# Performance work log

Measured on AMD Instinct MI355X. Metric: run time of the kernel, lower is better.

Reference implementation:

```python
import jax, jax.numpy as jnp
import numpy as np

KS = 3
N = KS * KS  # 9 kernel taps
EPS = 1e-5
LEAK = 0.1


def _conv2d(x, w, b=None, stride=1, pad=1):
    out = jax.lax.conv_general_dilated(
        x, w, (stride, stride), [(pad, pad), (pad, pad)],
        dimension_numbers=('NCHW', 'OIHW', 'NCHW'))
    if b is not None:
        out = out + b[None, :, None, None]
    return out


def setup_inputs() -> dict:
    key = jax.random.key(0)
    k1, k2, k3, k4 = jax.random.split(key, 4)
    b, c_in, c_out, H, W = 4, 128, 256, 128, 128
    x = jax.random.normal(k1, (b, c_in, H, W), dtype=jnp.float32)
    # offset-predicting conv (torch inits it to zero; small random keeps
    # sampling near-grid but nontrivial)
    p_w = jax.random.normal(k2, (2 * N, c_in, KS, KS), dtype=jnp.float32) * 0.01
    p_b = jnp.zeros((2 * N,), dtype=jnp.float32)
    # main conv weight (bias=False in DeformConv2d)
    w_conv = jax.random.normal(k3, (c_out, c_in, KS, KS), dtype=jnp.float32) * 0.05
    gamma = jnp.ones((c_out,), dtype=jnp.float32)
    beta = jnp.zeros((c_out,), dtype=jnp.float32)
    return {"x": x, "p_w": p_w, "p_b": p_b, "w_conv": w_conv,
            "gamma": gamma, "beta": beta}


def reference(x, p_w, p_b, w_conv, gamma, beta):
    b, c, H, W = x.shape
    # offsets: (b, 2N, H, W); first N channels = x-offsets, last N = y-offsets
    off = jnp.transpose(_conv2d(x, p_w, p_b), (0, 2, 3, 1))  # (b,h,w,2N)
    off_x, off_y = off[..., :N], off[..., N:]

    x_pad = jnp.pad(x, ((0, 0), (0, 0), (1, 1), (1, 1)))  # zero_padding(1)
    Hp, Wp = H + 2, W + 2

    # p = p_0 + p_n + offset (in padded coordinates)
    dx = jnp.repeat(jnp.arange(-1, 2), KS).astype(x.dtype)  # (9,)
    dy = jnp.tile(jnp.arange(-1, 2), KS).astype(x.dtype)
    p0x = jnp.arange(1, H + 1, dtype=x.dtype)[None, :, None, None]
    p0y = jnp.arange(1, W + 1, dtype=x.dtype)[None, None, :, None]
    px = p0x + dx + off_x  # (b,h,w,N)
    py = p0y + dy + off_y

    fx, fy = jnp.floor(px), jnp.floor(py)
    qlt_x = jnp.clip(fx, 0, Hp - 1)
    qlt_y = jnp.clip(fy, 0, Wp - 1)
    qrb_x = jnp.clip(fx + 1, 0, Hp - 1)
    qrb_y = jnp.clip(fy + 1, 0, Wp - 1)

    pcx = jnp.clip(px, 0, Hp - 1)
    pcy = jnp.clip(py, 0, Wp - 1)

    # bilinear weights (matches original g_lt/g_rb/g_lb/g_rt)
    g_lt = (1 + (qlt_x - pcx)) * (1 + (qlt_y - pcy))
    g_rb = (1 - (qrb_x - pcx)) * (1 - (qrb_y - pcy))
    g_lb = (1 + (qlt_x - pcx)) * (1 - (qrb_y - pcy))
    g_rt = (1 - (qrb_x - pcx)) * (1 + (qlt_y - pcy))

    x_flat = x_pad.reshape(b, c, Hp * Wp)
    ilt_x, ilt_y = qlt_x.astype(jnp.int32), qlt_y.astype(jnp.int32)
    irb_x, irb_y = qrb_x.astype(jnp.int32), qrb_y.astype(jnp.int32)

    def samp(ix, iy, g):
        idx = (ix * Wp + iy).reshape(b, -1)  # (b, h*w*N)
        v = jnp.take_along_axis(x_flat, idx[:, None, :], axis=2)
        return g[:, None] * v.reshape(b, c, H, W, N)

    x_off = (samp(ilt_x, ilt_y, g_lt) + samp(irb_x, irb_y, g_rb)
             + samp(ilt_x, irb_y, g_lb) + samp(irb_x, ilt_y, g_rt))

    # equivalent to reshaping to (b,c,3h,3w) and conv(k=3,s=3), bias=False
    out = jnp.einsum('bchwn,ocn->bohw', x_off,
                     w_conv.reshape(w_conv.shape[0], c, N))

    # BatchNorm2d (training-mode batch stats, biased var) + LeakyReLU(0.1)
    mean = out.mean(axis=(0, 2, 3), keepdims=True)
    var = ((out - mean) ** 2).mean(axis=(0, 2, 3), keepdims=True)
    out = (out - mean) * jax.lax.rsqrt(var + EPS)
    out = out * gamma[None, :, None, None] + beta[None, :, None, None]
    return jnp.where(out >= 0, out, LEAK * out)
```

## Files before the change

kernel.cpp:

```cpp
#include <hip/hip_runtime.h>
#include <cstdint>

typedef __attribute__((ext_vector_type(8))) short bf16x8;
typedef __attribute__((ext_vector_type(4))) float f32x4;

#define B_   4
#define C_   128
#define H_   128
#define W_   128
#define HP_  130
#define WP_  130
#define O_   256
#define HW_  (H_*W_)

#define XPAD_BYTES   (B_*HP_*WP_*C_*2)
#define OFF_BYTE     XPAD_BYTES
#define OFF_BYTES    (B_*HW_*18*4)
#define WREPB_BYTE   (OFF_BYTE + OFF_BYTES)
#define WREPB_BYTES  (9*C_*O_*2)
#define STATS_BYTE   (WREPB_BYTE + WREPB_BYTES)
#define WOFF_BYTE    (STATS_BYTE + 4096)
#define WOFF_BYTES   (9*4*4*32*8*2)
#define RAW_BYTE     (WOFF_BYTE + WOFF_BYTES)
#define RAW_BYTES    ((size_t)B_*O_*HW_*2)
#define WS_NEED      ((size_t)RAW_BYTE + RAW_BYTES)

typedef __attribute__((address_space(1))) const void gconst_void;
typedef __attribute__((address_space(3))) void lds_void;
#define GLD_LDS16(gp, lp) __builtin_amdgcn_global_load_lds((gconst_void*)(gp), (lds_void*)(lp), 16, 0, 0)

__device__ __forceinline__ unsigned pack_bf2(float a, float b) {
    unsigned ua = __builtin_bit_cast(unsigned, a) + 0x8000u;
    unsigned ub = __builtin_bit_cast(unsigned, b) + 0x8000u;
    return __builtin_amdgcn_perm(ub, ua, 0x07060302u);
}

__device__ __forceinline__ unsigned short bf16_rne(float f) {
    unsigned u = __builtin_bit_cast(unsigned, f);
    u += 0x7fffu + ((u >> 16) & 1u);
    return (unsigned short)(u >> 16);
}

__global__ void k_transpose(const float* __restrict__ x, unsigned short* __restrict__ xpad,
                            const float* __restrict__ p_w, short* __restrict__ wofff,
                            const float* __restrict__ w_conv, unsigned short* __restrict__ wrepb,
                            float* __restrict__ stats) {
    __shared__ float tile[32][33];
    int w0 = blockIdx.x * 32, c0 = blockIdx.y * 32;
    int bh = blockIdx.z;
    int b = bh >> 7, h = bh & 127;
    int tx = threadIdx.x, ty = threadIdx.y;
#pragma unroll
    for (int i = 0; i < 4; i++) {
        int c = c0 + ty + i * 8;
        tile[ty + i * 8][tx] = x[((b * C_ + c) * H_ + h) * W_ + w0 + tx];
    }
    int tid = ty * 32 + tx;
    {
        int fb = (bh * 4 + (int)blockIdx.y) * 4 + (int)blockIdx.x;
        int i = fb * 256 + tid;
        if (i < 1024) stats[i] = 0.f;
        if (i < 9 * 4096) {
            int e = i & 7, m = (i >> 3) & 31, q = (i >> 8) & 3, kc = (i >> 10) & 3, tap = i >> 12;
            float f = (m < 18) ? p_w[((size_t)m * C_ + kc * 32 + q * 8 + e) * 9 + tap] : 0.f;
            wofff[i] = (short)bf16_rne(f);
        }
        int j = i - 9 * 4096;
        if (j >= 0 && j < 9 * C_ * O_) {
            int ki8 = j & 7;
            int o   = (j >> 3) & 255;
            int kq  = (j >> 11) & 3;
            int kc  = (j >> 13) & 3;
            int n   = j >> 15;
            int c = kc * 32 + kq * 8 + ki8;
            wrepb[j] = bf16_rne(w_conv[(o * C_ + c) * 9 + n]);
        }
    }
    if (h == 0) {
        int wloc = tid >> 3, cq = tid & 7;
        size_t r0 = ((size_t)(b * HP_ + 0)   * WP_ + (w0 + 1 + wloc)) * C_ + c0 + cq * 4;
        size_t r1 = ((size_t)(b * HP_ + 129) * WP_ + (w0 + 1 + wloc)) * C_ + c0 + cq * 4;
        *(uint2*)&xpad[r0] = make_uint2(0u, 0u);
        *(uint2*)&xpad[r1] = make_uint2(0u, 0u);
        if (w0 == 0 && tid < 128) {
            int corner = tid >> 5, cc = tid & 31;
            int hp = (corner & 1) ? 129 : 0;
            int wp = (corner & 2) ? 129 : 0;
            xpad[((size_t)(b * HP_ + hp) * WP_ + wp) * C_ + c0 + cc] = 0;
        }
    }
    if (w0 == 0 && tid < 64) {
        int side = tid >> 5, cc = tid & 31;
        int wp = side ? 129 : 0;
        xpad[((size_t)(b * HP_ + h + 1) * WP_ + wp) * C_ + c0 + cc] = 0;
    }
    __syncthreads();
    if (tid < 128) {
        int w = tid >> 2, u4 = tid & 3;
        unsigned r0 = pack_bf2(tile[8 * u4 + 0][w], tile[8 * u4 + 1][w]);
        unsigned r1 = pack_bf2(tile[8 * u4 + 2][w], tile[8 * u4 + 3][w]);
        unsigned r2 = pack_bf2(tile[8 * u4 + 4][w], tile[8 * u4 + 5][w]);
        unsigned r3 = pack_bf2(tile[8 * u4 + 6][w], tile[8 * u4 + 7][w]);
        *(uint4*)&xpad[((size_t)((b * HP_ + h + 1) * WP_ + (w0 + w + 1))) * C_ + c0 + u4 * 8] =
            make_uint4(r0, r1, r2, r3);
    }
}

__global__ __launch_bounds__(256) void k_offconv(const unsigned short* __restrict__ xpad,
                                                 const short* __restrict__ wofff,
                                                 const float* __restrict__ p_b,
                                                 float* __restrict__ offT) {
    int t = threadIdx.x;
    int ph = blockIdx.x;
    int h  = blockIdx.y;
    int b  = blockIdx.z;
    const unsigned short* xb = xpad + (size_t)b * HP_ * WP_ * C_;
    int lane = t & 63, wv = t >> 6;
    int q = lane >> 4, l15 = lane & 15;
    int pos0 = ph * 64 + wv * 16;
    int poscol = pos0 + l15;

    f32x4 accA = {0.f, 0.f, 0.f, 0.f}, accB = {0.f, 0.f, 0.f, 0.f};
    const bf16x8* Wf = (const bf16x8*)wofff;

    for (int tap = 0; tap < 9; tap++) {
        int row = h + tap / 3;
        int col = poscol + tap % 3;
        const unsigned short* src = xb + ((size_t)(row * WP_ + col)) * C_ + q * 8;
#pragma unroll
        for (int kc = 0; kc < 4; kc++) {
            bf16x8 a0 = Wf[(size_t)(((tap * 4 + kc) * 4 + q) * 32) + l15];
            bf16x8 a1 = Wf[(size_t)(((tap * 4 + kc) * 4 + q) * 32) + 16 + l15];
            bf16x8 bv = *(const bf16x8*)(src + kc * 32);
            accA = __builtin_amdgcn_mfma_f32_16x16x32_bf16(a0, bv, accA, 0, 0, 0);
            accB = __builtin_amdgcn_mfma_f32_16x16x32_bf16(a1, bv, accB, 0, 0, 0);
        }
    }
    size_t hw = (size_t)h * W_ + pos0 + l15;
#pragma unroll
    for (int r = 0; r < 4; r++) {
        int j = q * 4 + r;
        offT[((size_t)(b * 18 + j)) * HW_ + hw] = accA[r] + p_b[j];
    }
    if (q == 0) {
#pragma unroll
        for (int r = 0; r < 2; r++) {
            int j = 16 + r;
            offT[((size_t)(b * 18 + j)) * HW_ + hw] = accB[r] + p_b[j];
        }
    }
}

__global__ __launch_bounds__(512, 4) void k_main(const unsigned short* __restrict__ xpad,
                                                 const float* __restrict__ offT,
                                                 const unsigned short* __restrict__ wrepb,
                                                 float* __restrict__ out,
                                                 float* __restrict__ stats,
                                                 unsigned short* __restrict__ rawout,
                                                 int bf16flag) {
    __shared__ short Wl[2][8192];
    __shared__ short Vl[2][4128];
    __shared__ int   pbase[2][4][128];
    __shared__ float pg[2][4][128];
    __shared__ float red0[256], red1[256];

    int t = threadIdx.x;
    int i_blk = blockIdx.x;
    int b = i_blk & 3;
    int h = i_blk >> 2;
    const unsigned short* xb = xpad + (size_t)b * HP_ * WP_ * C_;

    int lane = t & 63, wv = t >> 6;
    int q = lane >> 4, l15 = lane & 15;
    int m0 = (wv & 3) * 64;
    int ph = wv >> 2;
    int n0 = ph * 64;
    int c4g = t & 3, posb = t >> 2;

    auto OFFSETS = [&](int n, int pb) {
        if (t < 128) {
            int w = t;
            float offx = offT[((size_t)(b * 18 + n)) * HW_ + h * W_ + w];
            float offy = offT[((size_t)(b * 18 + 9 + n)) * HW_ + h * W_ + w];
            int dxn = n / 3 - 1, dyn = n % 3 - 1;
            float px = (float)(h + 1 + dxn) + offx;
            float py = (float)(w + 1 + dyn) + offy;
            float pcx = fminf(fmaxf(px, 0.f), 129.f);
            float pcy = fminf(fmaxf(py, 0.f), 129.f);
            float fx = floorf(px), fy = floorf(py);
            float q0x = fminf(fmaxf(fx, 0.f), 129.f);
            float q0y = fminf(fmaxf(fy, 0.f), 129.f);
            float q1x = fminf(fmaxf(fx + 1.f, 0.f), 129.f);
            float q1y = fminf(fmaxf(fy + 1.f, 0.f), 129.f);
            float wx0 = 1.f + (q0x - pcx), wx1 = 1.f - (q1x - pcx);
            float wy0 = 1.f + (q0y - pcy), wy1 = 1.f - (q1y - pcy);
            int i0x = (int)q0x, i0y = (int)q0y, i1x = (int)q1x, i1y = (int)q1y;
            pbase[pb][0][w] = (i0x * WP_ + i0y) * C_;
            pbase[pb][1][w] = (i1x * WP_ + i1y) * C_;
            pbase[pb][2][w] = (i0x * WP_ + i1y) * C_;
            pbase[pb][3][w] = (i1x * WP_ + i0y) * C_;
            pg[pb][0][w] = wx0 * wy0;
            pg[pb][1][w] = wx1 * wy1;
            pg[pb][2][w] = wx0 * wy1;
            pg[pb][3][w] = wx1 * wy0;
        }
    };

    f32x4 acc[4][4];
#pragma unroll
    for (int i = 0; i < 4; i++)
#pragma unroll
        for (int j = 0; j < 4; j++) acc[i][j] = (f32x4){0.f, 0.f, 0.f, 0.f};

    if (t < 256) { red0[t] = 0.f; red1[t] = 0.f; }
    OFFSETS(0, 0);
    __syncthreads();

    {
        const unsigned short* ws = wrepb;
        GLD_LDS16(ws + (size_t)t * 8, &Wl[0][wv * 512]);
        GLD_LDS16(ws + (size_t)(t + 512) * 8, &Wl[0][wv * 512 + 4096]);
        int cof = c4g * 8;
        uint4 A  = *(const uint4*)(xb + pbase[0][0][posb] + cof);
        uint4 Bv = *(const uint4*)(xb + pbase[0][1][posb] + cof);
        uint4 Cv = *(const uint4*)(xb + pbase[0][2][posb] + cof);
        uint4 Dv = *(const uint4*)(xb + pbase[0][3][posb] + cof);
        float g0 = pg[0][0][posb], g1 = pg[0][1][posb], g2 = pg[0][2][posb], g3 = pg[0][3][posb];
        unsigned outw[4];
#pragma unroll
        for (int k = 0; k < 4; k++) {
            unsigned ua = (&A.x)[k], ub = (&Bv.x)[k], uc = (&Cv.x)[k], ud = (&Dv.x)[k];
            float alo = __builtin_bit_cast(float, ua << 16), ahi = __builtin_bit_cast(float, ua & 0xffff0000u);
            float blo = __builtin_bit_cast(float, ub << 16), bhi = __builtin_bit_cast(float, ub & 0xffff0000u);
            float clo = __builtin_bit_cast(float, uc << 16), chi = __builtin_bit_cast(float, uc & 0xffff0000u);
            float dlo = __builtin_bit_cast(float, ud << 16), dhi = __builtin_bit_cast(float, ud & 0xffff0000u);
            float vlo = g0 * alo + g1 * blo + g2 * clo + g3 * dlo;
            float vhi = g0 * ahi + g1 * bhi + g2 * chi + g3 * dhi;
            outw[k] = pack_bf2(vlo, vhi);
        }
        *(uint4*)&Vl[0][(unsigned)(c4g * 129 + posb) * 8] = make_uint4(outw[0], outw[1], outw[2], outw[3]);
    }
    __syncthreads();

#pragma unroll 1
    for (int s = 0; s < 36; s++) {
        int cur = s & 1, nxt = cur ^ 1;
        uint4 A, Bv, Cv, Dv;
        float g0 = 0.f, g1 = 0.f, g2 = 0.f, g3 = 0.f;
        bool st = (s < 35);
        if (st) {
            int s1 = s + 1;
            const unsigned short* ws = wrepb + (size_t)s1 * 8192;
            GLD_LDS16(ws + (size_t)t * 8, &Wl[nxt][wv * 512]);
            GLD_LDS16(ws + (size_t)(t + 512) * 8, &Wl[nxt][wv * 512 + 4096]);
            int n1 = s1 >> 2, kc1 = s1 & 3, pb1 = n1 & 1;
            int cof = kc1 * 32 + c4g * 8;
            A  = *(const uint4*)(xb + pbase[pb1][0][posb] + cof);
            Bv = *(const uint4*)(xb + pbase[pb1][1][posb] + cof);
            Cv = *(const uint4*)(xb + pbase[pb1][2][posb] + cof);
            Dv = *(const uint4*)(xb + pbase[pb1][3][posb] + cof);
            g0 = pg[pb1][0][posb]; g1 = pg[pb1][1][posb];
            g2 = pg[pb1][2][posb]; g3 = pg[pb1][3][posb];
        }
        {
            const bf16x8* Af = (const bf16x8*)Wl[cur];
            const bf16x8* Bf = (const bf16x8*)Vl[cur];
            bf16x8 av[4];
#pragma unroll
            for (int i = 0; i < 4; i++) av[i] = Af[q * 256 + m0 + i * 16 + l15];
            __builtin_amdgcn_s_setprio(1);
#pragma unroll
            for (int j = 0; j < 4; j++) {
                bf16x8 bv = Bf[q * 129 + n0 + j * 16 + l15];
#pragma unroll
                for (int i = 0; i < 4; i++)
                    acc[i][j] = __builtin_amdgcn_mfma_f32_16x16x32_bf16(av[i], bv, acc[i][j], 0, 0, 0);
            }
            __builtin_amdgcn_s_setprio(0);
        }
        if ((s & 3) == 2) {
            int n = s >> 2;
            if (n < 8) OFFSETS(n + 1, (n + 1) & 1);
        }
        if (st) {
            unsigned outw[4];
#pragma unroll
            for (int k = 0; k < 4; k++) {
                unsigned ua = (&A.x)[k], ub = (&Bv.x)[k], uc = (&Cv.x)[k], ud = (&Dv.x)[k];
                float alo = __builtin_bit_cast(float, ua << 16), ahi = __builtin_bit_cast(float, ua & 0xffff0000u);
                float blo = __builtin_bit_cast(float, ub << 16), bhi = __builtin_bit_cast(float, ub & 0xffff0000u);
                float clo = __builtin_bit_cast(float, uc << 16), chi = __builtin_bit_cast(float, uc & 0xffff0000u);
                float dlo = __builtin_bit_cast(float, ud << 16), dhi = __builtin_bit_cast(float, ud & 0xffff0000u);
                float vlo = g0 * alo + g1 * blo + g2 * clo + g3 * dlo;
                float vhi = g0 * ahi + g1 * bhi + g2 * chi + g3 * dhi;
                outw[k] = pack_bf2(vlo, vhi);
            }
            *(uint4*)&Vl[nxt][(unsigned)(c4g * 129 + posb) * 8] = make_uint4(outw[0], outw[1], outw[2], outw[3]);
        }
        __syncthreads();
    }

#pragma unroll
    for (int i = 0; i < 4; i++) {
#pragma unroll
        for (int r = 0; r < 4; r++) {
            int o_loc = m0 + i * 16 + q * 4 + r;
            float s = 0.f, s2 = 0.f;
#pragma unroll
            for (int j = 0; j < 4; j++) { float v = acc[i][j][r]; s += v; s2 += v * v; }
            s  += __shfl_xor(s, 1);  s  += __shfl_xor(s, 2);  s  += __shfl_xor(s, 4);  s  += __shfl_xor(s, 8);
            s2 += __shfl_xor(s2, 1); s2 += __shfl_xor(s2, 2); s2 += __shfl_xor(s2, 4); s2 += __shfl_xor(s2, 8);
            if (l15 == 0) { atomicAdd(&red0[o_loc], s); atomicAdd(&red1[o_loc], s2); }
        }
    }
    __syncthreads();
    if (t < 256) {
        atomicAdd(&stats[t], red0[t]);
        atomicAdd(&stats[256 + t], red1[t]);
    }

    if (bf16flag) {
        unsigned short* rb = rawout + ((size_t)b * O_) * HW_ + (size_t)h * W_;
#pragma unroll
        for (int i = 0; i < 4; i++)
#pragma unroll
            for (int j = 0; j < 4; j++) {
                int col = ph * 64 + j * 16 + l15;
#pragma unroll
                for (int r = 0; r < 4; r++) {
                    int o = m0 + i * 16 + q * 4 + r;
                    rb[(size_t)o * HW_ + col] = bf16_rne(acc[i][j][r]);
                }
            }
    } else {
        float* outb = out + ((size_t)b * O_) * HW_ + (size_t)h * W_;
#pragma unroll
        for (int i = 0; i < 4; i++)
#pragma unroll
            for (int j = 0; j < 4; j++) {
                int col = ph * 64 + j * 16 + l15;
#pragma unroll
                for (int r = 0; r < 4; r++) {
                    int o = m0 + i * 16 + q * 4 + r;
                    outb[(size_t)o * HW_ + col] = acc[i][j][r];
                }
            }
    }
}

__global__ __launch_bounds__(256) void k_apply_bf16(const unsigned short* __restrict__ raw,
                                                    float* __restrict__ out,
                                                    const float* __restrict__ stats,
                                                    const float* __restrict__ gamma,
                                                    const float* __restrict__ beta) {
    size_t idx = (size_t)blockIdx.x * 256 + threadIdx.x;
    size_t e = idx * 8;
    int o = (int)((e >> 14) & 255);
    float s0 = stats[o], s2v = stats[256 + o];
    float mean = s0 * (1.f / 65536.f);
    float var = s2v * (1.f / 65536.f) - mean * mean;
    float sc = gamma[o] * rsqrtf(var + 1e-5f);
    float sh = beta[o] - mean * sc;
    uint4 rv = *(const uint4*)(raw + e);
    float vo[8];
#pragma unroll
    for (int k = 0; k < 4; k++) {
        unsigned w = (&rv.x)[k];
        vo[2 * k]     = __builtin_bit_cast(float, w << 16);
        vo[2 * k + 1] = __builtin_bit_cast(float, w & 0xffff0000u);
    }
#pragma unroll
    for (int k = 0; k < 8; k++) {
        float v = vo[k] * sc + sh;
        vo[k] = (v >= 0.f) ? v : 0.1f * v;
    }
    *(float4*)(out + e)     = make_float4(vo[0], vo[1], vo[2], vo[3]);
    *(float4*)(out + e + 4) = make_float4(vo[4], vo[5], vo[6], vo[7]);
}

__global__ __launch_bounds__(256) void k_apply_f32(float* __restrict__ out,
                                                   const float* __restrict__ stats,
                                                   const float* __restrict__ gamma,
                                                   const float* __restrict__ beta) {
    int idx = blockIdx.x * 256 + threadIdx.x;
    int e = idx * 4;
    int o = (e >> 14) & 255;
    float s0 = stats[o], s2v = stats[256 + o];
    float mean = s0 * (1.f / 65536.f);
    float var = s2v * (1.f / 65536.f) - mean * mean;
    float sc = gamma[o] * rsqrtf(var + 1e-5f);
    float sh = beta[o] - mean * sc;
    float4 v = *(float4*)(out + e);
    v.x = v.x * sc + sh; v.x = (v.x >= 0.f) ? v.x : 0.1f * v.x;
    v.y = v.y * sc + sh; v.y = (v.y >= 0.f) ? v.y : 0.1f * v.y;
    v.z = v.z * sc + sh; v.z = (v.z >= 0.f) ? v.z : 0.1f * v.z;
    v.w = v.w * sc + sh; v.w = (v.w >= 0.f) ? v.w : 0.1f * v.w;
    *(float4*)(out + e) = v;
}

extern "C" void kernel_launch(void* const* d_in, const int* in_sizes, int n_in,
                              void* d_out, int out_size, void* d_ws, size_t ws_size,
                              hipStream_t stream) {
    const float* x      = (const float*)d_in[0];
    const float* p_w    = (const float*)d_in[1];
    const float* p_b    = (const float*)d_in[2];
    const float* w_conv = (const float*)d_in[3];
    const float* gamma  = (const float*)d_in[4];
    const float* beta   = (const float*)d_in[5];
    float* out = (float*)d_out;

    char* wsb = (char*)d_ws;
    unsigned short* xpad  = (unsigned short*)wsb;
    float*          offT  = (float*)(wsb + OFF_BYTE);
    unsigned short* wrepb = (unsigned short*)(wsb + WREPB_BYTE);
    float*          stats = (float*)(wsb + STATS_BYTE);
    short*          wofff = (short*)(wsb + WOFF_BYTE);
    unsigned short* rawo  = (unsigned short*)(wsb + RAW_BYTE);

    int bf16flag = (ws_size >= WS_NEED) ? 1 : 0;

    k_transpose<<<dim3(W_ / 32, C_ / 32, B_ * H_), dim3(32, 8), 0, stream>>>(
        x, xpad, p_w, wofff, w_conv, wrepb, stats);
    k_offconv<<<dim3(2, H_, B_), 256, 0, stream>>>(xpad, wofff, p_b, offT);
    k_main<<<dim3(512), 512, 0, stream>>>(xpad, offT, wrepb, out, stats, rawo, bf16flag);
    if (bf16flag)
        k_apply_bf16<<<dim3(B_ * O_ * HW_ / (256 * 8)), 256, 0, stream>>>(rawo, out, stats, gamma, beta);
    else
        k_apply_f32<<<dim3(B_ * O_ * HW_ / (256 * 4)), 256, 0, stream>>>(out, stats, gamma, beta);
}
```

Baseline: 214.9 us.

## Fuse offset-prediction conv into main kernel and precompute packed sampling tables

```diff
diff --git a/kernel.cpp b/kernel.cpp
--- a/kernel.cpp
+++ b/kernel.cpp
@@ -1,4 +1,5 @@
 #include <hip/hip_runtime.h>
+#include <hip/hip_fp16.h>
 #include <cstdint>
 
 typedef __attribute__((ext_vector_type(8))) short bf16x8;
@@ -14,14 +15,12 @@
 #define HW_  (H_*W_)
 
 #define XPAD_BYTES   (B_*HP_*WP_*C_*2)
-#define OFF_BYTE     XPAD_BYTES
-#define OFF_BYTES    (B_*HW_*18*4)
-#define WREPB_BYTE   (OFF_BYTE + OFF_BYTES)
+#define WREPB_BYTE   XPAD_BYTES
 #define WREPB_BYTES  (9*C_*O_*2)
 #define STATS_BYTE   (WREPB_BYTE + WREPB_BYTES)
 #define WOFF_BYTE    (STATS_BYTE + 4096)
 #define WOFF_BYTES   (9*4*4*32*8*2)
-#define RAW_BYTE     (WOFF_BYTE + WOFF_BYTES)
+#define RAW_BYTE     ((WOFF_BYTE + WOFF_BYTES + 255) & ~255)
 #define RAW_BYTES    ((size_t)B_*O_*HW_*2)
 #define WS_NEED      ((size_t)RAW_BYTE + RAW_BYTES)
 
@@ -106,53 +105,9 @@
     }
 }
 
-__global__ __launch_bounds__(256) void k_offconv(const unsigned short* __restrict__ xpad,
+__global__ __launch_bounds__(512, 4) void k_main(const unsigned short* __restrict__ xpad,
                                                  const short* __restrict__ wofff,
                                                  const float* __restrict__ p_b,
-                                                 float* __restrict__ offT) {
-    int t = threadIdx.x;
-    int ph = blockIdx.x;
-    int h  = blockIdx.y;
-    int b  = blockIdx.z;
-    const unsigned short* xb = xpad + (size_t)b * HP_ * WP_ * C_;
-    int lane = t & 63, wv = t >> 6;
-    int q = lane >> 4, l15 = lane & 15;
-    int pos0 = ph * 64 + wv * 16;
-    int poscol = pos0 + l15;
-
-    f32x4 accA = {0.f, 0.f, 0.f, 0.f}, accB = {0.f, 0.f, 0.f, 0.f};
-    const bf16x8* Wf = (const bf16x8*)wofff;
-
-    for (int tap = 0; tap < 9; tap++) {
-        int row = h + tap / 3;
-        int col = poscol + tap % 3;
-        const unsigned short* src = xb + ((size_t)(row * WP_ + col)) * C_ + q * 8;
-#pragma unroll
-        for (int kc = 0; kc < 4; kc++) {
-            bf16x8 a0 = Wf[(size_t)(((tap * 4 + kc) * 4 + q) * 32) + l15];
-            bf16x8 a1 = Wf[(size_t)(((tap * 4 + kc) * 4 + q) * 32) + 16 + l15];
-            bf16x8 bv = *(const bf16x8*)(src + kc * 32);
-            accA = __builtin_amdgcn_mfma_f32_16x16x32_bf16(a0, bv, accA, 0, 0, 0);
-            accB = __builtin_amdgcn_mfma_f32_16x16x32_bf16(a1, bv, accB, 0, 0, 0);
-        }
-    }
-    size_t hw = (size_t)h * W_ + pos0 + l15;
-#pragma unroll
-    for (int r = 0; r < 4; r++) {
-        int j = q * 4 + r;
-        offT[((size_t)(b * 18 + j)) * HW_ + hw] = accA[r] + p_b[j];
-    }
-    if (q == 0) {
-#pragma unroll
-        for (int r = 0; r < 2; r++) {
-            int j = 16 + r;
-            offT[((size_t)(b * 18 + j)) * HW_ + hw] = accB[r] + p_b[j];
-        }
-    }
-}
-
-__global__ __launch_bounds__(512, 4) void k_main(const unsigned short* __restrict__ xpad,
-                                                 const float* __restrict__ offT,
                                                  const unsigned short* __restrict__ wrepb,
                                                  float* __restrict__ out,
                                                  float* __restrict__ stats,
@@ -160,9 +115,9 @@
                                                  int bf16flag) {
     __shared__ short Wl[2][8192];
     __shared__ short Vl[2][4128];
-    __shared__ int   pbase[2][4][128];
-    __shared__ float pg[2][4][128];
-    __shared__ float red0[256], red1[256];
+    __shared__ unsigned pbaseP[9][128];
+    __shared__ unsigned pg01[9][128];
+    __shared__ unsigned pg23[9][128];
 
     int t = threadIdx.x;
     int i_blk = blockIdx.x;
@@ -177,14 +132,47 @@
     int n0 = ph * 64;
     int c4g = t & 3, posb = t >> 2;
 
-    auto OFFSETS = [&](int n, int pb) {
-        if (t < 128) {
-            int w = t;
-            float offx = offT[((size_t)(b * 18 + n)) * HW_ + h * W_ + w];
-            float offy = offT[((size_t)(b * 18 + 9 + n)) * HW_ + h * W_ + w];
-            int dxn = n / 3 - 1, dyn = n % 3 - 1;
-            float px = (float)(h + 1 + dxn) + offx;
-            float py = (float)(w + 1 + dyn) + offy;
+    {
+        float* off_lds = (float*)&Wl[0][0];
+        f32x4 accA = {0.f, 0.f, 0.f, 0.f}, accB = {0.f, 0.f, 0.f, 0.f};
+        const bf16x8* Wf = (const bf16x8*)wofff;
+        int poscol = wv * 16 + l15;
+        for (int tap = 0; tap < 9; tap++) {
+            int row = h + tap / 3;
+            int col = poscol + tap % 3;
+            const unsigned short* src = xb + ((size_t)(row * WP_ + col)) * C_ + q * 8;
+#pragma unroll
+            for (int kc = 0; kc < 4; kc++) {
+                bf16x8 a0 = Wf[(size_t)(((tap * 4 + kc) * 4 + q) * 32) + l15];
+                bf16x8 a1 = Wf[(size_t)(((tap * 4 + kc) * 4 + q) * 32) + 16 + l15];
+                bf16x8 bv = *(const bf16x8*)(src + kc * 32);
+                accA = __builtin_amdgcn_mfma_f32_16x16x32_bf16(a0, bv, accA, 0, 0, 0);
+                accB = __builtin_amdgcn_mfma_f32_16x16x32_bf16(a1, bv, accB, 0, 0, 0);
+            }
+        }
+#pragma unroll
+        for (int r = 0; r < 4; r++) {
+            int j = q * 4 + r;
+            off_lds[j * 128 + poscol] = accA[r] + p_b[j];
+        }
+        if (q == 0) {
+#pragma unroll
+            for (int r = 0; r < 2; r++) {
+                int j = 16 + r;
+                off_lds[j * 128 + poscol] = accB[r] + p_b[j];
+            }
+        }
+    }
+    __syncthreads();
+    if (t < 128) {
+        const float* off_lds = (const float*)&Wl[0][0];
+        int w = t;
+#pragma unroll
+        for (int n = 0; n < 9; n++) {
+            float offx = off_lds[n * 128 + w];
+            float offy = off_lds[(9 + n) * 128 + w];
+            float px = (float)(h + n / 3) + offx;
+            float py = (float)(w + n % 3) + offy;
             float pcx = fminf(fmaxf(px, 0.f), 129.f);
             float pcy = fminf(fmaxf(py, 0.f), 129.f);
             float fx = floorf(px), fy = floorf(py);
@@ -194,16 +182,30 @@
             float q1y = fminf(fmaxf(fy + 1.f, 0.f), 129.f);
             float wx0 = 1.f + (q0x - pcx), wx1 = 1.f - (q1x - pcx);
             float wy0 = 1.f + (q0y - pcy), wy1 = 1.f - (q1y - pcy);
-            int i0x = (int)q0x, i0y = (int)q0y, i1x = (int)q1x, i1y = (int)q1y;
-            pbase[pb][0][w] = (i0x * WP_ + i0y) * C_;
-            pbase[pb][1][w] = (i1x * WP_ + i1y) * C_;
-            pbase[pb][2][w] = (i0x * WP_ + i1y) * C_;
-            pbase[pb][3][w] = (i1x * WP_ + i0y) * C_;
-            pg[pb][0][w] = wx0 * wy0;
-            pg[pb][1][w] = wx1 * wy1;
-            pg[pb][2][w] = wx0 * wy1;
-            pg[pb][3][w] = wx1 * wy0;
-        }
+            unsigned i0x = (unsigned)q0x, i0y = (unsigned)q0y;
+            unsigned i1x = (unsigned)q1x, i1y = (unsigned)q1y;
+            pbaseP[n][w] = i0x | (i0y << 8) | (i1x << 16) | (i1y << 24);
+            __half2 h01 = __floats2half2_rn(wx0 * wy0, wx1 * wy1);
+            __half2 h23 = __floats2half2_rn(wx0 * wy1, wx1 * wy0);
+            pg01[n][w] = __builtin_bit_cast(unsigned, h01);
+            pg23[n][w] = __builtin_bit_cast(unsigned, h23);
+        }
+    }
+    __syncthreads();
+
+    auto UNPACK = [&](int n, int& b0, int& b1, int& b2, int& b3,
+                      float& g0, float& g1, float& g2, float& g3) {
+        unsigned bp = pbaseP[n][posb];
+        int t0 = (int)(bp & 255u) * WP_;
+        int y0 = (int)((bp >> 8) & 255u);
+        int t1 = (int)((bp >> 16) & 255u) * WP_;
+        int y1 = (int)(bp >> 24);
+        b0 = (t0 + y0) * C_; b1 = (t1 + y1) * C_;
+        b2 = (t0 + y1) * C_; b3 = (t1 + y0) * C_;
+        __half2 h01 = __builtin_bit_cast(__half2, pg01[n][posb]);
+        __half2 h23 = __builtin_bit_cast(__half2, pg23[n][posb]);
+        g0 = __low2float(h01); g1 = __high2float(h01);
+        g2 = __low2float(h23); g3 = __high2float(h23);
     };
 
     f32x4 acc[4][4];
@@ -211,21 +213,18 @@
     for (int i = 0; i < 4; i++)
 #pragma unroll
         for (int j = 0; j < 4; j++) acc[i][j] = (f32x4){0.f, 0.f, 0.f, 0.f};
-
-    if (t < 256) { red0[t] = 0.f; red1[t] = 0.f; }
-    OFFSETS(0, 0);
-    __syncthreads();
 
     {
         const unsigned short* ws = wrepb;
         GLD_LDS16(ws + (size_t)t * 8, &Wl[0][wv * 512]);
         GLD_LDS16(ws + (size_t)(t + 512) * 8, &Wl[0][wv * 512 + 4096]);
+        int b0, b1, b2, b3; float g0, g1, g2, g3;
+        UNPACK(0, b0, b1, b2, b3, g0, g1, g2, g3);
         int cof = c4g * 8;
-        uint4 A  = *(const uint4*)(xb + pbase[0][0][posb] + cof);
-        uint4 Bv = *(const uint4*)(xb + pbase[0][1][posb] + cof);
-        uint4 Cv = *(const uint4*)(xb + pbase[0][2][posb] + cof);
-        uint4 Dv = *(const uint4*)(xb + pbase[0][3][posb] + cof);
-        float g0 = pg[0][0][posb], g1 = pg[0][1][posb], g2 = pg[0][2][posb], g3 = pg[0][3][posb];
+        uint4 A  = *(const uint4*)(xb + b0 + cof);
+        uint4 Bv = *(const uint4*)(xb + b1 + cof);
+        uint4 Cv = *(const uint4*)(xb + b2 + cof);
+        uint4 Dv = *(const uint4*)(xb + b3 + cof);
         unsigned outw[4];
 #pragma unroll
         for (int k = 0; k < 4; k++) {
@@ -253,14 +252,14 @@
             const unsigned short* ws = wrepb + (size_t)s1 * 8192;
             GLD_LDS16(ws + (size_t)t * 8, &Wl[nxt][wv * 512]);
             GLD_LDS16(ws + (size_t)(t + 512) * 8, &Wl[nxt][wv * 512 + 4096]);
-            int n1 = s1 >> 2, kc1 = s1 & 3, pb1 = n1 & 1;
+            int n1 = s1 >> 2, kc1 = s1 & 3;
+            int b0, b1, b2, b3;
+            UNPACK(n1, b0, b1, b2, b3, g0, g1, g2, g3);
             int cof = kc1 * 32 + c4g * 8;
-            A  = *(const uint4*)(xb + pbase[pb1][0][posb] + cof);
-            Bv = *(const uint4*)(xb + pbase[pb1][1][posb] + cof);
-            Cv = *(const uint4*)(xb + pbase[pb1][2][posb] + cof);
-            Dv = *(const uint4*)(xb + pbase[pb1][3][posb] + cof);
-            g0 = pg[pb1][0][posb]; g1 = pg[pb1][1][posb];
-            g2 = pg[pb1][2][posb]; g3 = pg[pb1][3][posb];
+            A  = *(const uint4*)(xb + b0 + cof);
+            Bv = *(const uint4*)(xb + b1 + cof);
+            Cv = *(const uint4*)(xb + b2 + cof);
+            Dv = *(const uint4*)(xb + b3 + cof);
         }
         {
             const bf16x8* Af = (const bf16x8*)Wl[cur];
@@ -277,10 +276,6 @@
                     acc[i][j] = __builtin_amdgcn_mfma_f32_16x16x32_bf16(av[i], bv, acc[i][j], 0, 0, 0);
             }
             __builtin_amdgcn_s_setprio(0);
-        }
-        if ((s & 3) == 2) {
-            int n = s >> 2;
-            if (n < 8) OFFSETS(n + 1, (n + 1) & 1);
         }
         if (st) {
             unsigned outw[4];
@@ -300,6 +295,10 @@
         __syncthreads();
     }
 
+    float* red0 = (float*)&Vl[0][0];
+    float* red1 = red0 + 256;
+    if (t < 256) { red0[t] = 0.f; red1[t] = 0.f; }
+    __syncthreads();
 #pragma unroll
     for (int i = 0; i < 4; i++) {
 #pragma unroll
@@ -411,7 +410,6 @@
 
     char* wsb = (char*)d_ws;
     unsigned short* xpad  = (unsigned short*)wsb;
-    float*          offT  = (float*)(wsb + OFF_BYTE);
     unsigned short* wrepb = (unsigned short*)(wsb + WREPB_BYTE);
     float*          stats = (float*)(wsb + STATS_BYTE);
     short*          wofff = (short*)(wsb + WOFF_BYTE);
@@ -421,8 +419,7 @@
 
     k_transpose<<<dim3(W_ / 32, C_ / 32, B_ * H_), dim3(32, 8), 0, stream>>>(
         x, xpad, p_w, wofff, w_conv, wrepb, stats);
-    k_offconv<<<dim3(2, H_, B_), 256, 0, stream>>>(xpad, wofff, p_b, offT);
-    k_main<<<dim3(512), 512, 0, stream>>>(xpad, offT, wrepb, out, stats, rawo, bf16flag);
+    k_main<<<dim3(512), 512, 0, stream>>>(xpad, wofff, p_b, wrepb, out, stats, rawo, bf16flag);
     if (bf16flag)
         k_apply_bf16<<<dim3(B_ * O_ * HW_ / (256 * 8)), 256, 0, stream>>>(rawo, out, stats, gamma, beta);
     else
```

Measured after the change: 211.0 us. About the same (-1.8%).
